# Kernel optimization log

Measured on AMD Instinct MI355X. Metric: run time of the kernel, lower is better.

The kernel has to match this reference:

```python
import jax, jax.numpy as jnp
import numpy as np

B, N, C_IN, H, S, K = 32, 1024, 2, 32, 2, 2  # batch, nodes, input feat, hidden, n_supports, k_hop
NUM_MAT = S * K + 1  # identity + K hops per support


def setup_inputs() -> dict:
    key = jax.random.key(0)
    ks = jax.random.split(key, 6)
    inputs = jax.random.normal(ks[0], (B, N, C_IN), dtype=jnp.float32)
    # dense diffusion supports, scaled ~1/N so k-hop products stay O(1) (row-stochastic-like)
    supports = jax.random.uniform(ks[1], (B, S, N, N), dtype=jnp.float32) * (2.0 / N)
    states = jax.random.normal(ks[2], (B, N, H), dtype=jnp.float32)
    c_cat = C_IN + H
    scale = 1.0 / np.sqrt(NUM_MAT * c_cat)
    W_ru = jax.random.normal(ks[3], (NUM_MAT * c_cat, 2 * H), dtype=jnp.float32) * scale
    b_ru = jnp.zeros((2 * H,), dtype=jnp.float32)
    W_c = jax.random.normal(ks[4], (NUM_MAT * c_cat, H), dtype=jnp.float32) * scale
    b_c = jnp.zeros((H,), dtype=jnp.float32)
    return {"inputs": inputs, "supports": supports, "states": states,
            "W_ru": W_ru, "b_ru": b_ru, "W_c": W_c, "b_c": b_c}


def _graph_conv(x, supports, W, b):
    # x: [B,N,C]; supports: [B,S,N,N]. DCRNN dense diffusion conv:
    feats = [x]
    for s in range(S):
        A = supports[:, s]  # [B,N,N]
        xk = x
        for _ in range(K):
            xk = jnp.einsum('bnm,bmc->bnc', A, xk)
            feats.append(xk)
    h = jnp.concatenate(feats, axis=-1)  # [B,N,NUM_MAT*C]
    return jnp.einsum('bnf,fo->bno', h, W) + b


def reference(inputs, supports, states, W_ru, b_ru, W_c, b_c):
    r_u = jax.nn.sigmoid(_graph_conv(jnp.concatenate([inputs, states], -1), supports, W_ru, b_ru))
    r, u = r_u[..., :H], r_u[..., H:]
    c = jnp.tanh(_graph_conv(jnp.concatenate([inputs, r * states], -1), supports, W_c, b_c))
    outputs = u * states + (1.0 - u) * c
    return (outputs, outputs)
```

## Files before the change

kernel.cpp:

```cpp
#include <hip/hip_runtime.h>


#define NN   1024
#define HB   245760
#define SUBT 16384
#define OUTCOPY 1048576
#define BUFSZ 38912

typedef float  f32x4  __attribute__((ext_vector_type(4)));
typedef short  s16x4  __attribute__((ext_vector_type(4)));
typedef short  s16x8  __attribute__((ext_vector_type(8)));
typedef __bf16 bf16x8 __attribute__((ext_vector_type(8)));
typedef unsigned int u32x4 __attribute__((ext_vector_type(4)));

#define GAS __attribute__((address_space(1)))
#define LAS __attribute__((address_space(3)))

__device__ __forceinline__ unsigned short f32_bf16(float f) {
  unsigned int u = __float_as_uint(f);
  u += 0x7FFFu + ((u >> 16) & 1u);
  return (unsigned short)(u >> 16);
}
__device__ __forceinline__ float bf16_f32(unsigned short h) {
  return __uint_as_float(((unsigned int)h) << 16);
}
__device__ __forceinline__ void gload_lds16(const unsigned short* g, void* l) {
  __builtin_amdgcn_global_load_lds((const GAS void*)g, (LAS void*)l, 16, 0, 0);
}

__global__ __launch_bounds__(256)
void cvt_bf16(const float* __restrict__ src, unsigned short* __restrict__ dst, int n4) {
  int i = blockIdx.x * 256 + threadIdx.x;
  int stride = gridDim.x * 256;
  for (; i < n4; i += stride) {
    float4 v = ((const float4*)src)[i];
    s16x4 o;
    o.x = (short)f32_bf16(v.x);
    o.y = (short)f32_bf16(v.y);
    o.z = (short)f32_bf16(v.z);
    o.w = (short)f32_bf16(v.w);
    ((s16x4*)dst)[i] = o;
  }
}

__global__ __launch_bounds__(256)
void pack_x1(const float* __restrict__ inputs, const float* __restrict__ states,
             unsigned short* __restrict__ H1) {
  int gid = blockIdx.x * 256 + threadIdx.x;
  int b = gid >> 10, n = gid & 1023;
  unsigned short* xb = H1 + (size_t)b * HB;
  xb[0 * NN + n] = f32_bf16(inputs[gid * 2 + 0]);
  xb[1 * NN + n] = f32_bf16(inputs[gid * 2 + 1]);
#pragma unroll
  for (int o = 0; o < 32; ++o) {
    int ch = 2 + o;
    xb[(ch >> 4) * SUBT + (ch & 15) * NN + n] = f32_bf16(states[gid * 32 + o]);
  }
#pragma unroll
  for (int ch = 34; ch < 48; ++ch)
    xb[2 * SUBT + (ch & 15) * NN + n] = 0;
}

__global__ __launch_bounds__(512, 2)
void hop_v3(const unsigned short* __restrict__ Abf,
            const unsigned short* __restrict__ Hin,
            unsigned short* __restrict__ Hout,
            int si0, int si1, int so0, int so1) {
  __shared__ u32x4 ldsv[3 * 2432];
  char* lds = (char*)ldsv;

  const int tid  = threadIdx.x;
  const int wave = tid >> 6, lane = tid & 63;
  const int l15  = lane & 15,  l4  = lane >> 4;
  const int mblk = blockIdx.x, b = blockIdx.y, s = blockIdx.z;
  const int slot_in  = s ? si1 : si0;
  const int slot_out = s ? so1 : so0;

  const unsigned short* Xb = Hin  + (size_t)b * HB + (size_t)slot_in  * 3 * SUBT;
  unsigned short*       Yb = Hout + (size_t)b * HB + (size_t)slot_out * 3 * SUBT;
  const size_t arow0 = ((size_t)(b * 2 + s) * NN + (size_t)mblk * 256) * NN;

  auto ISSUE = [&](int kt, char* base) {
    const int kb0 = kt << 6;
#pragma unroll
    for (int i = 0; i < 4; ++i) {
      int q = i * 512 + tid;
      int r = q >> 3, cs = q & 7;
      gload_lds16(Abf + arow0 + (size_t)r * NN + kb0 + ((cs ^ (r & 7)) << 3),
                  base + (i * 512 + wave * 64) * 16);
    }
    if (tid < 384) {
      int ct = tid >> 7, rem = tid & 127, ch = rem >> 3, cs = rem & 7;
      gload_lds16(Xb + ct * SUBT + ch * NN + kb0 + ((cs ^ (ch & 7)) << 3),
                  base + 32768 + (wave * 64) * 16);
    }
  };

  f32x4 acc[2][3];
#pragma unroll
  for (int mt = 0; mt < 2; ++mt)
#pragma unroll
    for (int nt = 0; nt < 3; ++nt)
#pragma unroll
      for (int e = 0; e < 4; ++e) acc[mt][nt][e] = 0.f;

  const int swx = (l15 & 7) << 4;

  auto COMPUTE = [&](const char* bc) {
    const char* lXb = bc + 32768;
#pragma unroll
    for (int kb = 0; kb < 2; ++kb) {
      const int ko = kb * 64 + (l4 << 3);
      bf16x8 afr[2];
#pragma unroll
      for (int mt = 0; mt < 2; ++mt) {
        int row = wave * 32 + mt * 16 + l15;
        int sw  = (row & 7) << 4;
        s16x8 t;
        t.lo = *(const s16x4*)(bc + row * 128 + (ko ^ sw));
        t.hi = *(const s16x4*)(bc + row * 128 + ((ko + 32) ^ sw));
        afr[mt] = __builtin_bit_cast(bf16x8, t);
      }
#pragma unroll
      for (int nt = 0; nt < 3; ++nt) {
        const char* bp = lXb + (nt * 16 + l15) * 128;
        s16x8 t;
        t.lo = *(const s16x4*)(bp + (ko ^ swx));
        t.hi = *(const s16x4*)(bp + ((ko + 32) ^ swx));
        bf16x8 bfr = __builtin_bit_cast(bf16x8, t);
#pragma unroll
        for (int mt = 0; mt < 2; ++mt)
          acc[mt][nt] = __builtin_amdgcn_mfma_f32_16x16x32_bf16(afr[mt], bfr, acc[mt][nt], 0, 0, 0);
      }
    }
  };

#define WB_MAIN() do {                                                   \
    if (wave < 6) asm volatile("s_waitcnt vmcnt(5)" ::: "memory");       \
    else          asm volatile("s_waitcnt vmcnt(4)" ::: "memory");       \
    __builtin_amdgcn_s_barrier();                                        \
    __builtin_amdgcn_sched_barrier(0);                                   \
  } while (0)
#define WB_LAST() do {                                                   \
    asm volatile("s_waitcnt vmcnt(0)" ::: "memory");                     \
    __builtin_amdgcn_s_barrier();                                        \
    __builtin_amdgcn_sched_barrier(0);                                   \
  } while (0)

  char* bA = lds;
  char* bB = lds + BUFSZ;
  char* bC = lds + 2 * BUFSZ;

  ISSUE(0, bA);
  ISSUE(1, bB);

#pragma unroll 1
  for (int kt = 0; kt < 14; ++kt) {
    WB_MAIN();
    ISSUE(kt + 2, bC);
    COMPUTE(bA);
    char* t = bA; bA = bB; bB = bC; bC = t;
  }
  WB_MAIN();  COMPUTE(bA);
  bA = bB;
  WB_LAST();  COMPUTE(bA);

#undef WB_MAIN
#undef WB_LAST

#pragma unroll
  for (int mt = 0; mt < 2; ++mt) {
    const int row0 = mblk * 256 + wave * 32 + mt * 16 + (l4 << 2);
#pragma unroll
    for (int nt = 0; nt < 3; ++nt) {
      int ch = nt * 16 + l15;
      s16x4 o;
      o.x = (short)f32_bf16(acc[mt][nt][0]);
      o.y = (short)f32_bf16(acc[mt][nt][1]);
      o.z = (short)f32_bf16(acc[mt][nt][2]);
      o.w = (short)f32_bf16(acc[mt][nt][3]);
      *(s16x4*)(Yb + (size_t)ch * NN + row0) = o;
    }
  }
}

__global__ __launch_bounds__(256)
void hop_slow(const float* __restrict__ Af32,
              const unsigned short* __restrict__ Hin,
              unsigned short* __restrict__ Hout,
              int si0, int si1, int so0, int so1) {
  __shared__ u32x4 lA4[1024];
  __shared__ u32x4 lX4[384];
  const int tid  = threadIdx.x;
  const int wave = tid >> 6, lane = tid & 63;
  const int l15  = lane & 15,  l4  = lane >> 4;
  const int mblk = blockIdx.x, b = blockIdx.y, s = blockIdx.z;
  const int slot_in  = s ? si1 : si0;
  const int slot_out = s ? so1 : so0;
  const unsigned short* Xb = Hin  + (size_t)b * HB + (size_t)slot_in  * 3 * SUBT;
  unsigned short*       Yb = Hout + (size_t)b * HB + (size_t)slot_out * 3 * SUBT;
  const size_t arow0 = ((size_t)(b * 2 + s) * NN + (size_t)mblk * 128) * NN;
  f32x4 acc[2][3];
#pragma unroll
  for (int mt = 0; mt < 2; ++mt)
#pragma unroll
    for (int nt = 0; nt < 3; ++nt)
#pragma unroll
      for (int e = 0; e < 4; ++e) acc[mt][nt][e] = 0.f;
  char* lAb = (char*)lA4;
  char* lXb = (char*)lX4;
  for (int kt = 0; kt < 16; ++kt) {
    const int kb0 = kt * 64;
    __syncthreads();
#pragma unroll
    for (int i = 0; i < 8; ++i) {
      int q = i * 256 + tid;
      int r = q >> 4, c = q & 15;
      float4 v = *(const float4*)(Af32 + arow0 + (size_t)r * NN + kb0 + c * 4);
      s16x4 o;
      o.x = (short)f32_bf16(v.x); o.y = (short)f32_bf16(v.y);
      o.z = (short)f32_bf16(v.z); o.w = (short)f32_bf16(v.w);
      *(s16x4*)(lAb + r * 128 + ((c * 8) ^ ((r & 7) << 4))) = o;
    }
    {
      int q = tid;
      int ct = q >> 7, rem = q & 127, ch = rem >> 3, c = rem & 7;
      const u32x4* src = (const u32x4*)(Xb + ct * SUBT + ch * NN + kb0 + c * 8);
      *(u32x4*)(lXb + ct * 2048 + ch * 128 + ((c ^ (ch & 7)) << 4)) = *src;
      if (tid < 128) {
        q = 256 + tid;
        ct = q >> 7; rem = q & 127; ch = rem >> 3; c = rem & 7;
        src = (const u32x4*)(Xb + ct * SUBT + ch * NN + kb0 + c * 8);
        *(u32x4*)(lXb + ct * 2048 + ch * 128 + ((c ^ (ch & 7)) << 4)) = *src;
      }
    }
    __syncthreads();
#pragma unroll
    for (int kb = 0; kb < 2; ++kb) {
      const int ko = kb * 64 + (l4 << 3);
      bf16x8 afr[2];
#pragma unroll
      for (int mt = 0; mt < 2; ++mt) {
        int row = wave * 32 + mt * 16 + l15;
        int sw  = (row & 7) << 4;
        s16x8 t;
        t.lo = *(const s16x4*)(lAb + row * 128 + (ko ^ sw));
        t.hi = *(const s16x4*)(lAb + row * 128 + ((ko + 32) ^ sw));
        afr[mt] = __builtin_bit_cast(bf16x8, t);
      }
#pragma unroll
      for (int nt = 0; nt < 3; ++nt) {
        const int swx = (l15 & 7) << 4;
        const char* bp = lXb + nt * 2048 + l15 * 128;
        s16x8 t;
        t.lo = *(const s16x4*)(bp + (ko ^ swx));
        t.hi = *(const s16x4*)(bp + ((ko + 32) ^ swx));
        bf16x8 bfr = __builtin_bit_cast(bf16x8, t);
#pragma unroll
        for (int mt = 0; mt < 2; ++mt)
          acc[mt][nt] = __builtin_amdgcn_mfma_f32_16x16x32_bf16(afr[mt], bfr, acc[mt][nt], 0, 0, 0);
      }
    }
  }
#pragma unroll
  for (int mt = 0; mt < 2; ++mt)
#pragma unroll
    for (int nt = 0; nt < 3; ++nt) {
      int ch   = nt * 16 + l15;
      int row0 = mblk * 128 + wave * 32 + mt * 16 + (l4 << 2);
      s16x4 o;
      o.x = (short)f32_bf16(acc[mt][nt][0]); o.y = (short)f32_bf16(acc[mt][nt][1]);
      o.z = (short)f32_bf16(acc[mt][nt][2]); o.w = (short)f32_bf16(acc[mt][nt][3]);
      *(s16x4*)(Yb + (size_t)ch * NN + row0) = o;
    }
}

__global__ __launch_bounds__(256)
void gate_ru_k(const unsigned short* __restrict__ H1,
               const float* __restrict__ W, const float* __restrict__ bias,
               const float* __restrict__ inputs, const float* __restrict__ states,
               unsigned short* __restrict__ H2, float* __restrict__ ubuf) {
  int gid = blockIdx.x * 256 + threadIdx.x;
  int b = gid >> 10, n = gid & 1023;
  const unsigned short* hb = H1 + (size_t)b * HB;
  float acc[64];
#pragma unroll
  for (int o = 0; o < 64; ++o) acc[o] = bias[o];
  for (int j = 0; j < 5; ++j) {
    const unsigned short* sb = hb + j * 3 * SUBT;
    for (int c = 0; c < 34; ++c) {
      float xv = bf16_f32(sb[(c >> 4) * SUBT + (c & 15) * NN + n]);
      const float* wr = W + (j * 34 + c) * 64;
#pragma unroll
      for (int o = 0; o < 64; ++o) acc[o] = fmaf(xv, wr[o], acc[o]);
    }
  }
  unsigned short* xb = H2 + (size_t)b * HB;
  xb[0 * NN + n] = f32_bf16(inputs[gid * 2 + 0]);
  xb[1 * NN + n] = f32_bf16(inputs[gid * 2 + 1]);
#pragma unroll
  for (int o = 0; o < 32; ++o) {
    float r = 1.f / (1.f + __expf(-acc[o]));
    float u = 1.f / (1.f + __expf(-acc[32 + o]));
    int ch = 2 + o;
    xb[(ch >> 4) * SUBT + (ch & 15) * NN + n] = f32_bf16(r * states[gid * 32 + o]);
    ubuf[((size_t)b * 32 + o) * NN + n] = u;
  }
#pragma unroll
  for (int ch = 34; ch < 48; ++ch)
    xb[2 * SUBT + (ch & 15) * NN + n] = 0;
}

__global__ __launch_bounds__(256)
void gate_c_k(const unsigned short* __restrict__ H2,
              const float* __restrict__ W, const float* __restrict__ bias,
              const float* __restrict__ states, const float* __restrict__ ubuf,
              float* __restrict__ out) {
  int gid = blockIdx.x * 256 + threadIdx.x;
  int b = gid >> 10, n = gid & 1023;
  const unsigned short* hb = H2 + (size_t)b * HB;
  float acc[32];
#pragma unroll
  for (int o = 0; o < 32; ++o) acc[o] = bias[o];
  for (int j = 0; j < 5; ++j) {
    const unsigned short* sb = hb + j * 3 * SUBT;
    for (int c = 0; c < 34; ++c) {
      float xv = bf16_f32(sb[(c >> 4) * SUBT + (c & 15) * NN + n]);
      const float* wr = W + (j * 34 + c) * 32;
#pragma unroll
      for (int o = 0; o < 32; ++o) acc[o] = fmaf(xv, wr[o], acc[o]);
    }
  }
  float res[32];
#pragma unroll
  for (int o = 0; o < 32; ++o) {
    float cc = tanhf(acc[o]);
    float u  = ubuf[((size_t)b * 32 + o) * NN + n];
    float sv = states[gid * 32 + o];
    res[o] = u * sv + (1.f - u) * cc;
  }
  float* o0 = out + (size_t)gid * 32;
#pragma unroll
  for (int q = 0; q < 8; ++q) {
    f32x4 v = { res[q * 4 + 0], res[q * 4 + 1], res[q * 4 + 2], res[q * 4 + 3] };
    *(f32x4*)(o0 + q * 4) = v;
    *(f32x4*)(o0 + OUTCOPY + q * 4) = v;
  }
}

extern "C" void kernel_launch(void* const* d_in, const int* in_sizes, int n_in,
                              void* d_out, int out_size, void* d_ws, size_t ws_size,
                              hipStream_t stream) {
  (void)in_sizes; (void)n_in; (void)out_size;
  const float* inputs   = (const float*)d_in[0];
  const float* supports = (const float*)d_in[1];
  const float* states   = (const float*)d_in[2];
  const float* W_ru     = (const float*)d_in[3];
  const float* b_ru     = (const float*)d_in[4];
  const float* W_c      = (const float*)d_in[5];
  const float* b_c      = (const float*)d_in[6];
  float* out = (float*)d_out;

  char* ws = (char*)d_ws;
  const size_t szA = 134217728;
  const size_t szH = 15728640;
  const size_t szU = 4194304;
  const bool pathA = ws_size >= szA + 2 * szH + szU;
  const size_t off = pathA ? szA : 0;

  unsigned short* Abf = (unsigned short*)ws;
  unsigned short* H1  = (unsigned short*)(ws + off);
  unsigned short* H2  = (unsigned short*)(ws + off + szH);
  float*          ub  = (float*)(ws + off + 2 * szH);

  dim3 vgrid(4, 32, 2), sgrid(8, 32, 2), blk256(256), blk512(512);

  if (pathA)
    cvt_bf16<<<dim3(2048), blk256, 0, stream>>>(supports, Abf, 16777216);

  pack_x1<<<dim3(128), blk256, 0, stream>>>(inputs, states, H1);

  if (pathA) {
    hop_v3<<<vgrid, blk512, 0, stream>>>(Abf, H1, H1, 0, 0, 1, 3);
    hop_v3<<<vgrid, blk512, 0, stream>>>(Abf, H1, H1, 1, 3, 2, 4);
  } else {
    hop_slow<<<sgrid, blk256, 0, stream>>>(supports, H1, H1, 0, 0, 1, 3);
    hop_slow<<<sgrid, blk256, 0, stream>>>(supports, H1, H1, 1, 3, 2, 4);
  }

  gate_ru_k<<<dim3(128), blk256, 0, stream>>>(H1, W_ru, b_ru, inputs, states, H2, ub);

  if (pathA) {
    hop_v3<<<vgrid, blk512, 0, stream>>>(Abf, H2, H2, 0, 0, 1, 3);
    hop_v3<<<vgrid, blk512, 0, stream>>>(Abf, H2, H2, 1, 3, 2, 4);
  } else {
    hop_slow<<<sgrid, blk256, 0, stream>>>(supports, H2, H2, 0, 0, 1, 3);
    hop_slow<<<sgrid, blk256, 0, stream>>>(supports, H2, H2, 1, 3, 2, 4);
  }

  gate_c_k<<<dim3(128), blk256, 0, stream>>>(H2, W_c, b_c, states, ub, out);
}
```

Baseline: 312.6 us.

## Pre-pack bf16 supports into tile-contiguous swizzled layout and stagger k-tile start

The fp32-to-bf16 conversion now writes the support matrices in a tile-major layout in which each 256x64 k-tile, already XOR-swizzled, is contiguous in memory. The hop kernel can then load each A tile with fully linear 16-byte global-to-LDS loads instead of strided row accesses. Each block also starts its k-loop at a different phase, which spreads concurrent accesses across memory channels. The conversion kernel's reads become strided gathers of 32-byte pieces, which may cost it some coalescing.

After: 323.6 us. 1.04x slower.

```diff
diff --git a/kernel.cpp b/kernel.cpp
--- a/kernel.cpp
+++ b/kernel.cpp
@@ -29,17 +29,26 @@
 }
 
 __global__ __launch_bounds__(256)
-void cvt_bf16(const float* __restrict__ src, unsigned short* __restrict__ dst, int n4) {
-  int i = blockIdx.x * 256 + threadIdx.x;
-  int stride = gridDim.x * 256;
-  for (; i < n4; i += stride) {
-    float4 v = ((const float4*)src)[i];
-    s16x4 o;
-    o.x = (short)f32_bf16(v.x);
-    o.y = (short)f32_bf16(v.y);
-    o.z = (short)f32_bf16(v.z);
-    o.w = (short)f32_bf16(v.w);
-    ((s16x4*)dst)[i] = o;
+void cvt_pack(const float* __restrict__ src, unsigned short* __restrict__ Apk) {
+  int g0 = blockIdx.x * 256 + threadIdx.x;
+#pragma unroll 1
+  for (int g = g0; g < 8388608; g += 524288) {
+    int c    = g & 2047;
+    int kt   = (g >> 11) & 15;
+    int mblk = (g >> 15) & 3;
+    int mat  = g >> 17;
+    int r = c >> 3, cs = c & 7;
+    int u = cs ^ (r & 7);
+    const float* p = src + ((size_t)mat << 20) + (size_t)(mblk * 256 + r) * 1024
+                         + kt * 64 + u * 8;
+    f32x4 v0 = *(const f32x4*)p;
+    f32x4 v1 = *(const f32x4*)(p + 4);
+    s16x8 o;
+    o[0] = (short)f32_bf16(v0[0]); o[1] = (short)f32_bf16(v0[1]);
+    o[2] = (short)f32_bf16(v0[2]); o[3] = (short)f32_bf16(v0[3]);
+    o[4] = (short)f32_bf16(v1[0]); o[5] = (short)f32_bf16(v1[1]);
+    o[6] = (short)f32_bf16(v1[2]); o[7] = (short)f32_bf16(v1[3]);
+    *(s16x8*)(Apk + (size_t)g * 8) = o;
   }
 }
 
@@ -62,7 +71,7 @@
 }
 
 __global__ __launch_bounds__(512, 2)
-void hop_v3(const unsigned short* __restrict__ Abf,
+void hop_v4(const unsigned short* __restrict__ Apk,
             const unsigned short* __restrict__ Hin,
             unsigned short* __restrict__ Hout,
             int si0, int si1, int so0, int so1) {
@@ -73,22 +82,22 @@
   const int wave = tid >> 6, lane = tid & 63;
   const int l15  = lane & 15,  l4  = lane >> 4;
   const int mblk = blockIdx.x, b = blockIdx.y, s = blockIdx.z;
+  const int mat  = b * 2 + s;
+  const int phase = (b + s * 8 + mblk * 4) & 15;
   const int slot_in  = s ? si1 : si0;
   const int slot_out = s ? so1 : so0;
 
   const unsigned short* Xb = Hin  + (size_t)b * HB + (size_t)slot_in  * 3 * SUBT;
   unsigned short*       Yb = Hout + (size_t)b * HB + (size_t)slot_out * 3 * SUBT;
-  const size_t arow0 = ((size_t)(b * 2 + s) * NN + (size_t)mblk * 256) * NN;
-
-  auto ISSUE = [&](int kt, char* base) {
-    const int kb0 = kt << 6;
-#pragma unroll
-    for (int i = 0; i < 4; ++i) {
-      int q = i * 512 + tid;
-      int r = q >> 3, cs = q & 7;
-      gload_lds16(Abf + arow0 + (size_t)r * NN + kb0 + ((cs ^ (r & 7)) << 3),
-                  base + (i * 512 + wave * 64) * 16);
-    }
+  const size_t tbase = (size_t)(mat * 4 + mblk) * 16 * 16384;
+
+  auto ISSUE = [&](int ktl, char* base) {
+    const int ktp = (ktl + phase) & 15;
+    const unsigned short* At = Apk + tbase + (size_t)ktp * 16384;
+    const int kb0 = ktp << 6;
+#pragma unroll
+    for (int i = 0; i < 4; ++i)
+      gload_lds16(At + (i * 512 + tid) * 8, base + (i * 512 + wave * 64) * 16);
     if (tid < 384) {
       int ct = tid >> 7, rem = tid & 127, ch = rem >> 3, cs = rem & 7;
       gload_lds16(Xb + ct * SUBT + ch * NN + kb0 + ((cs ^ (ch & 7)) << 3),
@@ -368,7 +377,7 @@
   const bool pathA = ws_size >= szA + 2 * szH + szU;
   const size_t off = pathA ? szA : 0;
 
-  unsigned short* Abf = (unsigned short*)ws;
+  unsigned short* Apk = (unsigned short*)ws;
   unsigned short* H1  = (unsigned short*)(ws + off);
   unsigned short* H2  = (unsigned short*)(ws + off + szH);
   float*          ub  = (float*)(ws + off + 2 * szH);
@@ -376,13 +385,13 @@
   dim3 vgrid(4, 32, 2), sgrid(8, 32, 2), blk256(256), blk512(512);
 
   if (pathA)
-    cvt_bf16<<<dim3(2048), blk256, 0, stream>>>(supports, Abf, 16777216);
+    cvt_pack<<<dim3(2048), blk256, 0, stream>>>(supports, Apk);
 
   pack_x1<<<dim3(128), blk256, 0, stream>>>(inputs, states, H1);
 
   if (pathA) {
-    hop_v3<<<vgrid, blk512, 0, stream>>>(Abf, H1, H1, 0, 0, 1, 3);
-    hop_v3<<<vgrid, blk512, 0, stream>>>(Abf, H1, H1, 1, 3, 2, 4);
+    hop_v4<<<vgrid, blk512, 0, stream>>>(Apk, H1, H1, 0, 0, 1, 3);
+    hop_v4<<<vgrid, blk512, 0, stream>>>(Apk, H1, H1, 1, 3, 2, 4);
   } else {
     hop_slow<<<sgrid, blk256, 0, stream>>>(supports, H1, H1, 0, 0, 1, 3);
     hop_slow<<<sgrid, blk256, 0, stream>>>(supports, H1, H1, 1, 3, 2, 4);
@@ -391,8 +400,8 @@
   gate_ru_k<<<dim3(128), blk256, 0, stream>>>(H1, W_ru, b_ru, inputs, states, H2, ub);
 
   if (pathA) {
-    hop_v3<<<vgrid, blk512, 0, stream>>>(Abf, H2, H2, 0, 0, 1, 3);
-    hop_v3<<<vgrid, blk512, 0, stream>>>(Abf, H2, H2, 1, 3, 2, 4);
+    hop_v4<<<vgrid, blk512, 0, stream>>>(Apk, H2, H2, 0, 0, 1, 3);
+    hop_v4<<<vgrid, blk512, 0, stream>>>(Apk, H2, H2, 1, 3, 2, 4);
   } else {
     hop_slow<<<sgrid, blk256, 0, stream>>>(supports, H2, H2, 0, 0, 1, 3);
     hop_slow<<<sgrid, blk256, 0, stream>>>(supports, H2, H2, 1, 3, 2, 4);
```
